# Optimization experiments

Measured on AMD Instinct MI355X. Metric: run time of the kernel, lower is better.

## Reference

```python
import jax, jax.numpy as jnp
import numpy as np


def _samx_row(qqq, kkk, vvv):
    """Suffix-automaton qkv retrieval over binary alphabet {0,1}.
    Faithful port of samx_qkv_slow, with dict transitions replaced by two
    flat transition arrays (alphabet size is 2 after the >0 binarization).
    """
    n = len(qqq)
    y = [0] * n
    s = 2 * n + 1
    tr = [[-1] * s, [-1] * s]   # tr[sym][state] = next state, -1 = absent
    f = [-1] * s                # suffix links
    m = [0] * s                 # max length of state
    r = [-1] * s                # last end position seen
    g = 0                       # last state
    u = 1                       # next free state id
    w = 0                       # current match state (query side)
    h = 0                       # current match length
    for i in range(n):
        q = qqq[i]
        k = kkk[i]
        tq = tr[q]
        tk = tr[k]
        # --- query: extend match with symbol q, following suffix links ---
        p, x = w, h
        while p != -1 and tq[p] == -1:
            if x > m[p]:
                x = m[p]
            p = f[p]
        if p != -1:
            p, x = tq[p], x + 1
        else:
            p, x = 0, 0
        # find tightest state for match length x
        vst = p
        while f[vst] != -1 and m[f[vst]] >= x:
            vst = f[vst]
        # back off to a state with positive length and a recorded endpos
        while vst != -1 and (m[vst] <= 0 or r[vst] < 0):
            vst = f[vst]
        yi = vvv[r[vst] + 1] if vst != -1 else -1
        y[i] = yi if yi > 0 else 0
        w, h = p, x
        # --- key: standard suffix-automaton extension with symbol k ---
        j = u
        u += 1
        m[j] = m[g] + 1
        p = g
        while p != -1 and tk[p] == -1:
            tk[p] = j
            p = f[p]
        if p == -1:
            f[j] = 0
        else:
            d = tk[p]
            if m[p] + 1 == m[d]:
                f[j] = d
            else:
                b = u
                u += 1
                tr[0][b] = tr[0][d]
                tr[1][b] = tr[1][d]
                m[b] = m[p] + 1
                f[b] = f[d]
                r[b] = r[d]
                f[d] = b
                f[j] = b
                while p != -1 and tk[p] == d:
                    tk[p] = b
                    p = f[p]
        # propagate latest end position up the suffix-link chain
        vst = g = j
        while vst != -1 and r[vst] < i:
            r[vst] = i
            vst = f[vst]
    return y


def _samx_idx(q, k, v):
    """q,k,v: float arrays [b,t,c] -> int idx [b,t,c] in {0,1}."""
    b, t, c = q.shape
    qb = (np.asarray(q) > 0).astype(np.uint8).transpose(0, 2, 1).reshape(-1, t)
    kb = (np.asarray(k) > 0).astype(np.uint8).transpose(0, 2, 1).reshape(-1, t)
    vb = (np.asarray(v) > 0).astype(np.uint8).transpose(0, 2, 1).reshape(-1, t)
    rows = [_samx_row(qq.tolist(), kk.tolist(), vv.tolist())
            for qq, kk, vv in zip(qb, kb, vb)]
    idx = np.asarray(rows, dtype=np.uint8).reshape(b, c, t).transpose(0, 2, 1)
    return idx


def setup_inputs() -> dict:
    key = jax.random.key(0)
    kq, kk, kv = jax.random.split(key, 3)
    B, T, C = 4, 2048, 256
    q = jax.random.normal(kq, (B, T, C), dtype=jnp.float32)
    k = jax.random.normal(kk, (B, T, C), dtype=jnp.float32)
    v = jax.random.normal(kv, (B, T, C), dtype=jnp.float32)
    e = jnp.ones((1, 1, C), dtype=jnp.float32)
    return {"q": q, "k": k, "v": v, "e": e}


def reference(q, k, v, e):
    # Irregular pointer-chasing part runs on host (numpy); output scaling in jnp.
    idx = _samx_idx(q, k, v)                      # [b,t,c] in {0,1}
    sign = 2.0 * jnp.asarray(idx, dtype=q.dtype) - 1.0
    return sign * e
```

## Files before the change

### kernel.cpp

```cpp
#include <hip/hip_runtime.h>


#define NSTATES 4096
#define TLEN 2048

typedef unsigned long long u64m;

__device__ __forceinline__ int f_tr(u64m r, int s) {
  return (int)(short)(unsigned short)(r >> (s << 4));
}
__device__ __forceinline__ int f_fl(u64m r) {
  return (int)(short)(unsigned short)(r >> 32);
}
__device__ __forceinline__ int f_ml(u64m r) {
  return (int)(r >> 48);
}

__device__ __forceinline__ int lane_shr1(int v, int lane) {
  int sh = __builtin_amdgcn_update_dpp(0, v, 0x111 , 0xF, 0xF, true);
  const int v15 = __builtin_amdgcn_readlane(v, 15);
  const int v31 = __builtin_amdgcn_readlane(v, 31);
  const int v47 = __builtin_amdgcn_readlane(v, 47);
  if (lane == 16) sh = v15;
  if (lane == 32) sh = v31;
  if (lane == 48) sh = v47;
  return sh;
}

__global__ __launch_bounds__(128)
void samx_main(const float* __restrict__ q,
               const float* __restrict__ k,
               unsigned* __restrict__ outpos,
               int T, int C) {
  __shared__ u64m           reca[NSTATES];
  __shared__ unsigned short rla[NSTATES];

  unsigned short* recw = (unsigned short*)reca;
  unsigned*       rech = (unsigned*)reca;

  const int row = blockIdx.x;
  const int b = row / C;
  const int c = row - b * C;
  const int lane = threadIdx.x & 63;
  const int wid = threadIdx.x >> 6;

  for (int s = threadIdx.x; s < NSTATES; s += 128) {
    reca[s] = 0x0000FFFFFFFFFFFFull;
    rla[s] = 0xFFFFu;
  }

  const size_t rowbase = (size_t)b * (size_t)T * (size_t)C + (size_t)c;
  unsigned* outr = outpos + rowbase;

  const float* src = (wid == 0 ? k : q) + rowbase;
  unsigned bits = 0u;
  {
    const int t0 = lane * 32;
#pragma unroll 8
    for (int jj = 0; jj < 32; ++jj) {
      if (src[(size_t)(t0 + jj) * C] > 0.0f) bits |= (1u << jj);
    }
  }
  __syncthreads();

  int cid = 0;
  bool cval = (lane == 0);
  bool trunc = false;
  int g = 0;
  int mlg = 0;
  int u = 1;
  int w = 0;
  int h = 0;

  int sym = (int)(__builtin_amdgcn_readlane((int)bits, 0) & 1);

  for (int i = 0; i < T; ++i) {
    const bool hot = !trunc;
    const int j = u++;
    const int mlj = mlg + 1;

    int d = -1, bb = -1, flj = 0, ndd = 0, newlen = 2, pushed = 0;
    bool prefl = false, inrun = false;

    if (wid == 0) {
      if (hot) {
        const int ks = sym;
        const u64m rk = reca[cid];
        const int img = f_tr(rk, ks);
        const int myml = f_ml(rk);
        const u64m brkmask = __ballot(cval && img != -1);
        const bool nobrk = (brkmask == 0);
        const int t2 = nobrk ? 64 : (int)__builtin_ctzll(brkmask);
        const int t2c = (t2 > 63) ? 63 : t2;
        d = __builtin_amdgcn_readlane(img, t2c);
        const int mlp = __builtin_amdgcn_readlane(myml, t2c);
        prefl = cval && (lane < t2);

        const u64m recd = reca[d < 0 ? 0 : d];

        const int previmg = lane_shr1(img, lane);
        const bool rs = cval && lane >= t2 && (lane == t2 || img != previmg);
        const u64m rsmask = __ballot(rs);
        ndd = (int)__builtin_popcountll(rsmask);
        newlen = ndd + 2;
        const unsigned below =
            __builtin_amdgcn_mbcnt_hi((unsigned)(rsmask >> 32),
                __builtin_amdgcn_mbcnt_lo((unsigned)rsmask, 0u));
        const int dst = rs ? ((int)below + 1) : 0;
        pushed = __builtin_amdgcn_ds_permute(dst << 2, img);

        int dtr0 = f_tr(recd, 0);
        int dtr1 = f_tr(recd, 1);
        const unsigned fmdhi = (unsigned)(recd >> 32);
        if (!nobrk) {
          const int mld = (int)(fmdhi >> 16);
          if (mlp + 1 == mld) {
            flj = d;
          } else {
            bb = u++;
            const u64m pb = __ballot(prefl && cid == d);
            if (pb != 0ull) { if (ks) dtr1 = j; else dtr0 = j; }
            if (lane == 0) {
              reca[bb] = (u64m)(unsigned short)dtr0
                       | ((u64m)(unsigned short)dtr1 << 16)
                       | ((u64m)(fmdhi & 0xFFFFu) << 32)
                       | ((u64m)(unsigned)(mlp + 1) << 48);
            }
            flj = bb;
          }
        }
        if (lane == 0)
          rech[2 * j + 1] = (unsigned)(flj & 0xFFFF) | ((unsigned)mlj << 16);

        if (bb >= 0) {
          const u64m eq = __ballot(cval && img == d) >> t2;
          const int runlen = (eq == ~0ull) ? 64 : (int)__builtin_ctzll(~eq);
          inrun = cval && lane >= t2 && lane < t2 + runlen;
        }
      }
    } else {
      const int qs = sym;
      int p = w, x = h;
      {
        u64m rr = reca[w];
        for (;;) {
          const int tv = f_tr(rr, qs);
          if (tv != -1) { p = tv; x = x + 1; break; }
          const int mp = f_ml(rr);
          if (x > mp) x = mp;
          p = f_fl(rr);
          if (p == -1) { p = 0; x = 0; break; }
          rr = reca[p];
        }
      }
      const u64m recP = reca[p];
      int rlv = (int)(short)rla[p];
      unsigned fmv = (unsigned)(recP >> 32);
      int vst = p;
      for (;;) {
        const int fv = (int)(short)(fmv & 0xFFFFu);
        if (fv == -1) break;
        const unsigned fmf = rech[2 * fv + 1];
        const int rlf = (int)(short)rla[fv];
        if ((int)(fmf >> 16) < x) break;
        vst = fv; fmv = fmf; rlv = rlf;
      }
      int rv = -1;
      for (;;) {
        if (vst == -1) { rv = -1; break; }
        if ((int)(fmv >> 16) > 0 && rlv >= 0) { rv = rlv; break; }
        vst = (int)(short)(fmv & 0xFFFFu);
        if (vst == -1) { rv = -1; break; }
        fmv = rech[2 * vst + 1];
        rlv = (int)(short)rla[vst];
      }
      w = p; h = x;
      if (lane == 0) outr[(size_t)i * C] = (unsigned)(rv + 1);
    }

    asm volatile("" ::: "memory");
    __builtin_amdgcn_s_barrier();
    asm volatile("" ::: "memory");

    if (wid == 0) {
      const int ks = sym;
      if (hot) {
        if (prefl) recw[4 * cid + ks] = (unsigned short)j;
        if (inrun) recw[4 * cid + ks] = (unsigned short)bb;
        if (bb >= 0 && lane == 0) recw[4 * d + 2] = (unsigned short)bb;

        int nv = 0;
        if (lane == 0) nv = j;
        else if (lane == 1) nv = flj;
        else if (lane - 1 < ndd) nv = pushed;
        const bool nval = (lane < newlen);
        if (nval) rla[nv] = (unsigned short)i;

        const bool overflow = (newlen > 64);
        if (overflow) {
          const int nv63 = __builtin_amdgcn_readlane(nv, 63);
          if (lane == 0) {
            int vp = (int)(short)(rech[2 * nv63 + 1] & 0xFFFFu);
            while (vp != -1) {
              rla[vp] = (unsigned short)i;
              vp = (int)(short)(rech[2 * vp + 1] & 0xFFFFu);
            }
          }
        }
        cid = nv; cval = nval; trunc = overflow;
      } else {
        int pcur = g, d2 = -1, idbrk = -1;
        for (;;) {
          if (pcur == -1) break;
          const u64m rr = reca[pcur];
          const int tv = f_tr(rr, ks);
          if (tv != -1) { d2 = tv; idbrk = pcur; break; }
          if (lane == 0) recw[4 * pcur + ks] = (unsigned short)j;
          pcur = f_fl(rr);
        }
        int fl2 = 0;
        if (d2 != -1) {
          const int mlp2 = f_ml(reca[idbrk]);
          const u64m rd2 = reca[d2];
          const int mld = f_ml(rd2);
          if (mlp2 + 1 == mld) {
            fl2 = d2;
          } else {
            const int bbc = u++;
            const int drl = (int)(short)rla[d2];
            if (lane == 0) {
              reca[bbc] = (u64m)(unsigned short)f_tr(rd2, 0)
                        | ((u64m)(unsigned short)f_tr(rd2, 1) << 16)
                        | ((u64m)((unsigned)(rd2 >> 32) & 0xFFFFu) << 32)
                        | ((u64m)(unsigned)(mlp2 + 1) << 48);
              rla[bbc] = (unsigned short)drl;
              recw[4 * d2 + 2] = (unsigned short)bbc;
            }
            fl2 = bbc;
            int p3 = idbrk;
            for (;;) {
              if (p3 == -1) break;
              const u64m r3 = reca[p3];
              const int tv3 = f_tr(r3, ks);
              if (tv3 != d2) break;
              if (lane == 0) recw[4 * p3 + ks] = (unsigned short)bbc;
              p3 = f_fl(r3);
            }
          }
        }
        if (lane == 0)
          rech[2 * j + 1] = (unsigned)(fl2 & 0xFFFF) | ((unsigned)mlj << 16);
        int vp = j, ncs = 0;
        bool tr2 = false;
        for (;;) {
          if (vp == -1) break;
          if (ncs < 64) { if (lane == ncs) cid = vp; ++ncs; }
          else tr2 = true;
          if (lane == 0) rla[vp] = (unsigned short)i;
          vp = (int)(short)(rech[2 * vp + 1] & 0xFFFFu);
        }
        cval = (lane < ncs);
        trunc = tr2;
      }
      g = j; mlg = mlj;
    }

    if (i + 1 < T) {
      const int in = i + 1;
      const unsigned bw = (unsigned)__builtin_amdgcn_readlane((int)bits, in >> 5);
      sym = (int)((bw >> (in & 31)) & 1u);
    }

    asm volatile("s_waitcnt lgkmcnt(0)" ::: "memory");
    __builtin_amdgcn_s_barrier();
    asm volatile("" ::: "memory");
  }
}

__global__ __launch_bounds__(256)
void samx_epilogue(const float* __restrict__ v,
                   const float* __restrict__ e,
                   unsigned* __restrict__ out,
                   int T, int C, int total) {
  const int idx = blockIdx.x * 256 + threadIdx.x;
  if (idx >= total) return;
  const unsigned vidx = out[idx];
  const int c = idx % C;
  const int bi = idx / C;
  const int b = bi / T;
  const float ev = e[c];
  float val = -ev;
  if (vidx != 0u) {
    if (v[((size_t)b * (size_t)T + (size_t)vidx) * (size_t)C + (size_t)c] > 0.0f)
      val = ev;
  }
  out[idx] = __float_as_uint(val);
}

extern "C" void kernel_launch(void* const* d_in, const int* in_sizes, int n_in,
                              void* d_out, int out_size, void* d_ws, size_t ws_size,
                              hipStream_t stream) {
  const float* q = (const float*)d_in[0];
  const float* k = (const float*)d_in[1];
  const float* v = (const float*)d_in[2];
  const float* e = (const float*)d_in[3];

  const int C = in_sizes[3];
  const int T = TLEN;
  const int B = in_sizes[0] / (T * C);
  const int total = out_size;

  samx_main<<<dim3(B * C), dim3(128), 0, stream>>>(q, k, (unsigned*)d_out, T, C);
  samx_epilogue<<<dim3((total + 255) / 256), dim3(256), 0, stream>>>(
      v, e, (unsigned*)d_out, T, C, total);
}
```

Measured before the change: 1.577 ms.

## Prefetch next-step automaton records and short-circuit break search via lane-1 record

The key wave now loads the next iteration's state record for its chain before the barrier, and keeps a register copy of the root state (rec0). When lane 1's successor record is known, it takes the transition break directly from that record, skipping the ballot/readlane search and the dependent LDS read of the break target. This aims to cut the serialized LDS latency on the per-step critical path. In exchange it adds extra register state and tracking logic that must stay consistent with the shared-memory records, especially after a clone or in the truncated (overflow) path.

```diff
diff --git a/kernel.cpp b/kernel.cpp
--- a/kernel.cpp
+++ b/kernel.cpp
@@ -14,6 +14,10 @@
 }
 __device__ __forceinline__ int f_ml(u64m r) {
   return (int)(r >> 48);
+}
+__device__ __forceinline__ u64m set_tr(u64m r, int s, int v) {
+  const int sh = s << 4;
+  return (r & ~(0xFFFFull << sh)) | ((u64m)(unsigned short)v << sh);
 }
 
 __device__ __forceinline__ int lane_shr1(int v, int lane) {
@@ -69,6 +73,12 @@
   int g = 0;
   int mlg = 0;
   int u = 1;
+  u64m rec0 = 0x0000FFFFFFFFFFFFull;
+  u64m pf_rec = reca[0];
+  u64m pf1c = 0;
+  u64m pf_recd = 0;
+  int  nx1 = -1;
+  bool have_pf1 = false;
   int w = 0;
   int h = 0;
 
@@ -80,23 +90,29 @@
     const int mlj = mlg + 1;
 
     int d = -1, bb = -1, flj = 0, ndd = 0, newlen = 2, pushed = 0;
-    bool prefl = false, inrun = false;
+    bool prefl = false, inrun = false, nobrk = false;
+    u64m pf1pre = 0;
 
     if (wid == 0) {
       if (hot) {
         const int ks = sym;
-        const u64m rk = reca[cid];
+        const u64m rk = pf_rec;
         const int img = f_tr(rk, ks);
-        const int myml = f_ml(rk);
-        const u64m brkmask = __ballot(cval && img != -1);
-        const bool nobrk = (brkmask == 0);
-        const int t2 = nobrk ? 64 : (int)__builtin_ctzll(brkmask);
-        const int t2c = (t2 > 63) ? 63 : t2;
-        d = __builtin_amdgcn_readlane(img, t2c);
-        const int mlp = __builtin_amdgcn_readlane(myml, t2c);
+        int t2, mlp;
+        u64m recd;
+        if (nx1 >= 0) {
+          t2 = 1; d = nx1; mlp = f_ml(pf1c); recd = pf_recd;
+        } else {
+          const int myml = f_ml(rk);
+          const u64m brkmask = __ballot(cval && img != -1);
+          nobrk = (brkmask == 0);
+          t2 = nobrk ? 64 : (int)__builtin_ctzll(brkmask);
+          const int t2c = (t2 > 63) ? 63 : t2;
+          d = __builtin_amdgcn_readlane(img, t2c);
+          mlp = __builtin_amdgcn_readlane(myml, t2c);
+          recd = reca[d < 0 ? 0 : d];
+        }
         prefl = cval && (lane < t2);
-
-        const u64m recd = reca[d < 0 ? 0 : d];
 
         const int previmg = lane_shr1(img, lane);
         const bool rs = cval && lane >= t2 && (lane == t2 || img != previmg);
@@ -116,15 +132,20 @@
           const int mld = (int)(fmdhi >> 16);
           if (mlp + 1 == mld) {
             flj = d;
+            pf1pre = (u64m)(unsigned short)dtr0
+                   | ((u64m)(unsigned short)dtr1 << 16)
+                   | ((u64m)(fmdhi & 0xFFFFu) << 32)
+                   | ((u64m)(unsigned)mld << 48);
           } else {
             bb = u++;
             const u64m pb = __ballot(prefl && cid == d);
             if (pb != 0ull) { if (ks) dtr1 = j; else dtr0 = j; }
+            pf1pre = (u64m)(unsigned short)dtr0
+                   | ((u64m)(unsigned short)dtr1 << 16)
+                   | ((u64m)(fmdhi & 0xFFFFu) << 32)
+                   | ((u64m)(unsigned)(mlp + 1) << 48);
             if (lane == 0) {
-              reca[bb] = (u64m)(unsigned short)dtr0
-                       | ((u64m)(unsigned short)dtr1 << 16)
-                       | ((u64m)(fmdhi & 0xFFFFu) << 32)
-                       | ((u64m)(unsigned)(mlp + 1) << 48);
+              reca[bb] = pf1pre;
             }
             flj = bb;
           }
@@ -182,12 +203,18 @@
     __builtin_amdgcn_s_barrier();
     asm volatile("" ::: "memory");
 
+    u64m pf1n = 0;
     if (wid == 0) {
       const int ks = sym;
       if (hot) {
         if (prefl) recw[4 * cid + ks] = (unsigned short)j;
         if (inrun) recw[4 * cid + ks] = (unsigned short)bb;
         if (bb >= 0 && lane == 0) recw[4 * d + 2] = (unsigned short)bb;
+
+        if (nobrk) rec0 = set_tr(rec0, ks, j);
+        else if (bb >= 0 && __ballot(inrun && cid == 0) != 0ull)
+          rec0 = set_tr(rec0, ks, bb);
+        pf1n = nobrk ? rec0 : pf1pre;
 
         int nv = 0;
         if (lane == 0) nv = j;
@@ -208,6 +235,7 @@
           }
         }
         cid = nv; cval = nval; trunc = overflow;
+        have_pf1 = !overflow;
       } else {
         int pcur = g, d2 = -1, idbrk = -1;
         for (;;) {
@@ -261,6 +289,8 @@
         }
         cval = (lane < ncs);
         trunc = tr2;
+        rec0 = reca[0];
+        have_pf1 = false;
       }
       g = j; mlg = mlj;
     }
@@ -271,7 +301,15 @@
       sym = (int)((bw >> (in & 31)) & 1u);
     }
 
-    asm volatile("s_waitcnt lgkmcnt(0)" ::: "memory");
+    if (wid == 0) {
+      asm volatile("s_waitcnt lgkmcnt(0)" ::: "memory");
+      if (i + 1 < T) {
+        pf_rec = reca[cid];
+        nx1 = have_pf1 ? f_tr(pf1n, sym) : -1;
+        pf_recd = reca[nx1 < 0 ? 0 : nx1];
+        pf1c = pf1n;
+      }
+    }
     __builtin_amdgcn_s_barrier();
     asm volatile("" ::: "memory");
   }
```

Measured after the change: 1.890 ms. 19.8% more time.

## Interleave two suffix-automaton rows per block with prefetched state records

Applied to the files above, without the earlier changes.

Each block now processes two independent rows in lock-step, with duplicated shared-memory automata, so the per-step barrier and LDS latency chains of one row overlap with the other's. It also prefetches the key-side current state record before the barrier, and adds a fast path on the query side that reuses the previously loaded record when it has not changed. The grid is halved. This doubles LDS use per block, which may lower occupancy, and relies on B*C being even.

```diff
diff --git a/kernel.cpp b/kernel.cpp
--- a/kernel.cpp
+++ b/kernel.cpp
@@ -32,150 +32,192 @@
                const float* __restrict__ k,
                unsigned* __restrict__ outpos,
                int T, int C) {
-  __shared__ u64m           reca[NSTATES];
-  __shared__ unsigned short rla[NSTATES];
-
-  unsigned short* recw = (unsigned short*)reca;
-  unsigned*       rech = (unsigned*)reca;
-
-  const int row = blockIdx.x;
-  const int b = row / C;
-  const int c = row - b * C;
+  __shared__ u64m           reca[2][NSTATES];
+  __shared__ unsigned short rla[2][NSTATES];
+
+  unsigned short* recwv[2] = {(unsigned short*)&reca[0][0],
+                              (unsigned short*)&reca[1][0]};
+  unsigned*       rechv[2] = {(unsigned*)&reca[0][0],
+                              (unsigned*)&reca[1][0]};
+
   const int lane = threadIdx.x & 63;
   const int wid = threadIdx.x >> 6;
 
   for (int s = threadIdx.x; s < NSTATES; s += 128) {
-    reca[s] = 0x0000FFFFFFFFFFFFull;
-    rla[s] = 0xFFFFu;
+    reca[0][s] = 0x0000FFFFFFFFFFFFull;
+    reca[1][s] = 0x0000FFFFFFFFFFFFull;
+    rla[0][s] = 0xFFFFu;
+    rla[1][s] = 0xFFFFu;
   }
 
-  const size_t rowbase = (size_t)b * (size_t)T * (size_t)C + (size_t)c;
-  unsigned* outr = outpos + rowbase;
-
-  const float* src = (wid == 0 ? k : q) + rowbase;
-  unsigned bits = 0u;
+  size_t rowbase[2];
+  unsigned* outr[2];
+  unsigned bits[2] = {0u, 0u};
   {
-    const int t0 = lane * 32;
+    const float* srcb = (wid == 0) ? k : q;
+#pragma unroll
+    for (int r = 0; r < 2; ++r) {
+      const int row = blockIdx.x * 2 + r;
+      const int b = row / C;
+      const int c = row - b * C;
+      rowbase[r] = (size_t)b * (size_t)T * (size_t)C + (size_t)c;
+      outr[r] = outpos + rowbase[r];
+      const float* src = srcb + rowbase[r];
+      const int t0 = lane * 32;
 #pragma unroll 8
-    for (int jj = 0; jj < 32; ++jj) {
-      if (src[(size_t)(t0 + jj) * C] > 0.0f) bits |= (1u << jj);
+      for (int jj = 0; jj < 32; ++jj) {
+        if (src[(size_t)(t0 + jj) * C] > 0.0f) bits[r] |= (1u << jj);
+      }
     }
   }
   __syncthreads();
 
-  int cid = 0;
-  bool cval = (lane == 0);
-  bool trunc = false;
-  int g = 0;
-  int mlg = 0;
-  int u = 1;
-  int w = 0;
-  int h = 0;
-
-  int sym = (int)(__builtin_amdgcn_readlane((int)bits, 0) & 1);
+  int  cid[2]  = {0, 0};
+  bool cval[2] = {lane == 0, lane == 0};
+  bool trunc[2] = {false, false};
+  int  g[2] = {0, 0}, mlg[2] = {0, 0}, uu[2] = {1, 1};
+  u64m pf_rec[2] = {reca[0][0], reca[1][0]};
+  int  w[2] = {0, 0}, h[2] = {0, 0};
+  u64m rrP[2] = {reca[0][0], reca[1][0]};
+
+  int symv[2];
+#pragma unroll
+  for (int r = 0; r < 2; ++r)
+    symv[r] = (int)(__builtin_amdgcn_readlane((int)bits[r], 0) & 1);
 
   for (int i = 0; i < T; ++i) {
-    const bool hot = !trunc;
-    const int j = u++;
-    const int mlj = mlg + 1;
-
-    int d = -1, bb = -1, flj = 0, ndd = 0, newlen = 2, pushed = 0;
-    bool prefl = false, inrun = false;
+    bool hot[2]; int jj[2], mljv[2];
+#pragma unroll
+    for (int r = 0; r < 2; ++r) {
+      hot[r] = !trunc[r];
+      jj[r] = uu[r]++;
+      mljv[r] = mlg[r] + 1;
+    }
+
+    int d[2] = {-1, -1}, bb[2] = {-1, -1}, flj[2] = {0, 0};
+    int ndd[2] = {0, 0}, newlen[2] = {2, 2}, pushed[2] = {0, 0};
+    int t2v[2] = {64, 64}, mlp[2] = {0, 0}, imgv[2] = {-1, -1};
+    bool prefl[2] = {false, false}, inrun[2] = {false, false};
+    bool nobrk[2] = {false, false};
+    u64m recd[2] = {0, 0};
 
     if (wid == 0) {
-      if (hot) {
-        const int ks = sym;
-        const u64m rk = reca[cid];
-        const int img = f_tr(rk, ks);
+#pragma unroll
+      for (int r = 0; r < 2; ++r) if (hot[r]) {
+        const int ks = symv[r];
+        const u64m rk = pf_rec[r];
+        imgv[r] = f_tr(rk, ks);
         const int myml = f_ml(rk);
-        const u64m brkmask = __ballot(cval && img != -1);
-        const bool nobrk = (brkmask == 0);
-        const int t2 = nobrk ? 64 : (int)__builtin_ctzll(brkmask);
-        const int t2c = (t2 > 63) ? 63 : t2;
-        d = __builtin_amdgcn_readlane(img, t2c);
-        const int mlp = __builtin_amdgcn_readlane(myml, t2c);
-        prefl = cval && (lane < t2);
-
-        const u64m recd = reca[d < 0 ? 0 : d];
-
-        const int previmg = lane_shr1(img, lane);
-        const bool rs = cval && lane >= t2 && (lane == t2 || img != previmg);
+        const u64m brkmask = __ballot(cval[r] && imgv[r] != -1);
+        nobrk[r] = (brkmask == 0);
+        t2v[r] = nobrk[r] ? 64 : (int)__builtin_ctzll(brkmask);
+        const int t2c = (t2v[r] > 63) ? 63 : t2v[r];
+        d[r] = __builtin_amdgcn_readlane(imgv[r], t2c);
+        mlp[r] = __builtin_amdgcn_readlane(myml, t2c);
+        prefl[r] = cval[r] && (lane < t2v[r]);
+
+        recd[r] = reca[r][d[r] < 0 ? 0 : d[r]];
+
+        const int previmg = lane_shr1(imgv[r], lane);
+        const bool rs = cval[r] && lane >= t2v[r] &&
+                        (lane == t2v[r] || imgv[r] != previmg);
         const u64m rsmask = __ballot(rs);
-        ndd = (int)__builtin_popcountll(rsmask);
-        newlen = ndd + 2;
+        ndd[r] = (int)__builtin_popcountll(rsmask);
+        newlen[r] = ndd[r] + 2;
         const unsigned below =
             __builtin_amdgcn_mbcnt_hi((unsigned)(rsmask >> 32),
                 __builtin_amdgcn_mbcnt_lo((unsigned)rsmask, 0u));
         const int dst = rs ? ((int)below + 1) : 0;
-        pushed = __builtin_amdgcn_ds_permute(dst << 2, img);
-
-        int dtr0 = f_tr(recd, 0);
-        int dtr1 = f_tr(recd, 1);
-        const unsigned fmdhi = (unsigned)(recd >> 32);
-        if (!nobrk) {
+        pushed[r] = __builtin_amdgcn_ds_permute(dst << 2, imgv[r]);
+      }
+#pragma unroll
+      for (int r = 0; r < 2; ++r) if (hot[r]) {
+        const int ks = symv[r];
+        int dtr0 = f_tr(recd[r], 0);
+        int dtr1 = f_tr(recd[r], 1);
+        const unsigned fmdhi = (unsigned)(recd[r] >> 32);
+        if (!nobrk[r]) {
           const int mld = (int)(fmdhi >> 16);
-          if (mlp + 1 == mld) {
-            flj = d;
+          if (mlp[r] + 1 == mld) {
+            flj[r] = d[r];
           } else {
-            bb = u++;
-            const u64m pb = __ballot(prefl && cid == d);
-            if (pb != 0ull) { if (ks) dtr1 = j; else dtr0 = j; }
+            bb[r] = uu[r]++;
+            const u64m pb = __ballot(prefl[r] && cid[r] == d[r]);
+            if (pb != 0ull) { if (ks) dtr1 = jj[r]; else dtr0 = jj[r]; }
             if (lane == 0) {
-              reca[bb] = (u64m)(unsigned short)dtr0
-                       | ((u64m)(unsigned short)dtr1 << 16)
-                       | ((u64m)(fmdhi & 0xFFFFu) << 32)
-                       | ((u64m)(unsigned)(mlp + 1) << 48);
+              reca[r][bb[r]] = (u64m)(unsigned short)dtr0
+                             | ((u64m)(unsigned short)dtr1 << 16)
+                             | ((u64m)(fmdhi & 0xFFFFu) << 32)
+                             | ((u64m)(unsigned)(mlp[r] + 1) << 48);
             }
-            flj = bb;
+            flj[r] = bb[r];
           }
         }
         if (lane == 0)
-          rech[2 * j + 1] = (unsigned)(flj & 0xFFFF) | ((unsigned)mlj << 16);
-
-        if (bb >= 0) {
-          const u64m eq = __ballot(cval && img == d) >> t2;
+          rechv[r][2 * jj[r] + 1] =
+              (unsigned)(flj[r] & 0xFFFF) | ((unsigned)mljv[r] << 16);
+
+        if (bb[r] >= 0) {
+          const u64m eq = __ballot(cval[r] && imgv[r] == d[r]) >> t2v[r];
           const int runlen = (eq == ~0ull) ? 64 : (int)__builtin_ctzll(~eq);
-          inrun = cval && lane >= t2 && lane < t2 + runlen;
+          inrun[r] = cval[r] && lane >= t2v[r] && lane < t2v[r] + runlen;
         }
       }
     } else {
-      const int qs = sym;
-      int p = w, x = h;
-      {
-        u64m rr = reca[w];
+      u64m fresh[2], rr2[2]; int rl2[2], tvs[2];
+#pragma unroll
+      for (int r = 0; r < 2; ++r) {
+        const int qs = symv[r];
+        fresh[r] = reca[r][w[r]];
+        tvs[r] = f_tr(rrP[r], qs);
+        const int ps = (tvs[r] != -1) ? tvs[r] : 0;
+        rr2[r] = reca[r][ps];
+        rl2[r] = (int)(short)rla[r][ps];
+      }
+#pragma unroll
+      for (int r = 0; r < 2; ++r) {
+        const int qs = symv[r];
+        int p, x;
+        u64m recP; int rlv;
+        if (fresh[r] == rrP[r] && tvs[r] != -1) {
+          p = tvs[r]; x = h[r] + 1; recP = rr2[r]; rlv = rl2[r];
+        } else {
+          u64m rr = fresh[r]; p = w[r]; x = h[r];
+          for (;;) {
+            const int tv = f_tr(rr, qs);
+            if (tv != -1) { p = tv; x = x + 1; break; }
+            const int mp = f_ml(rr);
+            if (x > mp) x = mp;
+            p = f_fl(rr);
+            if (p == -1) { p = 0; x = 0; break; }
+            rr = reca[r][p];
+          }
+          recP = reca[r][p]; rlv = (int)(short)rla[r][p];
+        }
+
+        unsigned fmv = (unsigned)(recP >> 32);
+        int vst = p;
         for (;;) {
-          const int tv = f_tr(rr, qs);
-          if (tv != -1) { p = tv; x = x + 1; break; }
-          const int mp = f_ml(rr);
-          if (x > mp) x = mp;
-          p = f_fl(rr);
-          if (p == -1) { p = 0; x = 0; break; }
-          rr = reca[p];
-        }
-      }
-      const u64m recP = reca[p];
-      int rlv = (int)(short)rla[p];
-      unsigned fmv = (unsigned)(recP >> 32);
-      int vst = p;
-      for (;;) {
-        const int fv = (int)(short)(fmv & 0xFFFFu);
-        if (fv == -1) break;
-        const unsigned fmf = rech[2 * fv + 1];
-        const int rlf = (int)(short)rla[fv];
-        if ((int)(fmf >> 16) < x) break;
-        vst = fv; fmv = fmf; rlv = rlf;
-      }
-      int rv = -1;
-      for (;;) {
-        if (vst == -1) { rv = -1; break; }
-        if ((int)(fmv >> 16) > 0 && rlv >= 0) { rv = rlv; break; }
-        vst = (int)(short)(fmv & 0xFFFFu);
-        if (vst == -1) { rv = -1; break; }
-        fmv = rech[2 * vst + 1];
-        rlv = (int)(short)rla[vst];
-      }
-      w = p; h = x;
-      if (lane == 0) outr[(size_t)i * C] = (unsigned)(rv + 1);
+          const int fv = (int)(short)(fmv & 0xFFFFu);
+          if (fv == -1) break;
+          const unsigned fmf = rechv[r][2 * fv + 1];
+          const int rlf = (int)(short)rla[r][fv];
+          if ((int)(fmf >> 16) < x) break;
+          vst = fv; fmv = fmf; rlv = rlf;
+        }
+        int rv = -1;
+        for (;;) {
+          if (vst == -1) { rv = -1; break; }
+          if ((int)(fmv >> 16) > 0 && rlv >= 0) { rv = rlv; break; }
+          vst = (int)(short)(fmv & 0xFFFFu);
+          if (vst == -1) { rv = -1; break; }
+          fmv = rechv[r][2 * vst + 1];
+          rlv = (int)(short)rla[r][vst];
+        }
+        w[r] = p; h[r] = x;
+        rrP[r] = recP;
+        if (lane == 0) outr[r][(size_t)i * C] = (unsigned)(rv + 1);
+      }
     }
 
     asm volatile("" ::: "memory");
@@ -183,95 +225,108 @@
     asm volatile("" ::: "memory");
 
     if (wid == 0) {
-      const int ks = sym;
-      if (hot) {
-        if (prefl) recw[4 * cid + ks] = (unsigned short)j;
-        if (inrun) recw[4 * cid + ks] = (unsigned short)bb;
-        if (bb >= 0 && lane == 0) recw[4 * d + 2] = (unsigned short)bb;
-
-        int nv = 0;
-        if (lane == 0) nv = j;
-        else if (lane == 1) nv = flj;
-        else if (lane - 1 < ndd) nv = pushed;
-        const bool nval = (lane < newlen);
-        if (nval) rla[nv] = (unsigned short)i;
-
-        const bool overflow = (newlen > 64);
-        if (overflow) {
-          const int nv63 = __builtin_amdgcn_readlane(nv, 63);
-          if (lane == 0) {
-            int vp = (int)(short)(rech[2 * nv63 + 1] & 0xFFFFu);
-            while (vp != -1) {
-              rla[vp] = (unsigned short)i;
-              vp = (int)(short)(rech[2 * vp + 1] & 0xFFFFu);
+#pragma unroll
+      for (int r = 0; r < 2; ++r) {
+        const int ks = symv[r];
+        if (hot[r]) {
+          if (prefl[r]) recwv[r][4 * cid[r] + ks] = (unsigned short)jj[r];
+          if (inrun[r]) recwv[r][4 * cid[r] + ks] = (unsigned short)bb[r];
+          if (bb[r] >= 0 && lane == 0)
+            recwv[r][4 * d[r] + 2] = (unsigned short)bb[r];
+
+          int nv = 0;
+          if (lane == 0) nv = jj[r];
+          else if (lane == 1) nv = flj[r];
+          else if (lane - 1 < ndd[r]) nv = pushed[r];
+          const bool nval = (lane < newlen[r]);
+          if (nval) rla[r][nv] = (unsigned short)i;
+
+          const bool overflow = (newlen[r] > 64);
+          if (overflow) {
+            const int nv63 = __builtin_amdgcn_readlane(nv, 63);
+            if (lane == 0) {
+              int vp = (int)(short)(rechv[r][2 * nv63 + 1] & 0xFFFFu);
+              while (vp != -1) {
+                rla[r][vp] = (unsigned short)i;
+                vp = (int)(short)(rechv[r][2 * vp + 1] & 0xFFFFu);
+              }
             }
           }
-        }
-        cid = nv; cval = nval; trunc = overflow;
-      } else {
-        int pcur = g, d2 = -1, idbrk = -1;
-        for (;;) {
-          if (pcur == -1) break;
-          const u64m rr = reca[pcur];
-          const int tv = f_tr(rr, ks);
-          if (tv != -1) { d2 = tv; idbrk = pcur; break; }
-          if (lane == 0) recw[4 * pcur + ks] = (unsigned short)j;
-          pcur = f_fl(rr);
-        }
-        int fl2 = 0;
-        if (d2 != -1) {
-          const int mlp2 = f_ml(reca[idbrk]);
-          const u64m rd2 = reca[d2];
-          const int mld = f_ml(rd2);
-          if (mlp2 + 1 == mld) {
-            fl2 = d2;
-          } else {
-            const int bbc = u++;
-            const int drl = (int)(short)rla[d2];
-            if (lane == 0) {
-              reca[bbc] = (u64m)(unsigned short)f_tr(rd2, 0)
-                        | ((u64m)(unsigned short)f_tr(rd2, 1) << 16)
-                        | ((u64m)((unsigned)(rd2 >> 32) & 0xFFFFu) << 32)
-                        | ((u64m)(unsigned)(mlp2 + 1) << 48);
-              rla[bbc] = (unsigned short)drl;
-              recw[4 * d2 + 2] = (unsigned short)bbc;
+          cid[r] = nv; cval[r] = nval; trunc[r] = overflow;
+        } else {
+          int pcur = g[r], d2 = -1, idbrk = -1;
+          for (;;) {
+            if (pcur == -1) break;
+            const u64m rr = reca[r][pcur];
+            const int tv = f_tr(rr, ks);
+            if (tv != -1) { d2 = tv; idbrk = pcur; break; }
+            if (lane == 0) recwv[r][4 * pcur + ks] = (unsigned short)jj[r];
+            pcur = f_fl(rr);
+          }
+          int fl2 = 0;
+          if (d2 != -1) {
+            const int mlp2 = f_ml(reca[r][idbrk]);
+            const u64m rd2 = reca[r][d2];
+            const int mld = f_ml(rd2);
+            if (mlp2 + 1 == mld) {
+              fl2 = d2;
+            } else {
+              const int bbc = uu[r]++;
+              const int drl = (int)(short)rla[r][d2];
+              if (lane == 0) {
+                reca[r][bbc] = (u64m)(unsigned short)f_tr(rd2, 0)
+                             | ((u64m)(unsigned short)f_tr(rd2, 1) << 16)
+                             | ((u64m)((unsigned)(rd2 >> 32) & 0xFFFFu) << 32)
+                             | ((u64m)(unsigned)(mlp2 + 1) << 48);
+                rla[r][bbc] = (unsigned short)drl;
+                recwv[r][4 * d2 + 2] = (unsigned short)bbc;
+              }
+              fl2 = bbc;
+              int p3 = idbrk;
+              for (;;) {
+                if (p3 == -1) break;
+                const u64m r3 = reca[r][p3];
+                const int tv3 = f_tr(r3, ks);
+                if (tv3 != d2) break;
+                if (lane == 0) recwv[r][4 * p3 + ks] = (unsigned short)bbc;
+                p3 = f_fl(r3);
+              }
             }
-            fl2 = bbc;
-            int p3 = idbrk;
-            for (;;) {
-              if (p3 == -1) break;
-              const u64m r3 = reca[p3];
-              const int tv3 = f_tr(r3, ks);
-              if (tv3 != d2) break;
-              if (lane == 0) recw[4 * p3 + ks] = (unsigned short)bbc;
-              p3 = f_fl(r3);
-            }
-          }
-        }
-        if (lane == 0)
-          rech[2 * j + 1] = (unsigned)(fl2 & 0xFFFF) | ((unsigned)mlj << 16);
-        int vp = j, ncs = 0;
-        bool tr2 = false;
-        for (;;) {
-          if (vp == -1) break;
-          if (ncs < 64) { if (lane == ncs) cid = vp; ++ncs; }
-          else tr2 = true;
-          if (lane == 0) rla[vp] = (unsigned short)i;
-          vp = (int)(short)(rech[2 * vp + 1] & 0xFFFFu);
-        }
-        cval = (lane < ncs);
-        trunc = tr2;
-      }
-      g = j; mlg = mlj;
+          }
+          if (lane == 0)
+            rechv[r][2 * jj[r] + 1] =
+                (unsigned)(fl2 & 0xFFFF) | ((unsigned)mljv[r] << 16);
+          int vp = jj[r], ncs = 0;
+          bool tr2 = false;
+          for (;;) {
+            if (vp == -1) break;
+            if (ncs < 64) { if (lane == ncs) cid[r] = vp; ++ncs; }
+            else tr2 = true;
+            if (lane == 0) rla[r][vp] = (unsigned short)i;
+            vp = (int)(short)(rechv[r][2 * vp + 1] & 0xFFFFu);
+          }
+          cval[r] = (lane < ncs);
+          trunc[r] = tr2;
+        }
+        g[r] = jj[r]; mlg[r] = mljv[r];
+      }
     }
 
     if (i + 1 < T) {
       const int in = i + 1;
-      const unsigned bw = (unsigned)__builtin_amdgcn_readlane((int)bits, in >> 5);
-      sym = (int)((bw >> (in & 31)) & 1u);
+#pragma unroll
+      for (int r = 0; r < 2; ++r) {
+        const unsigned bw =
+            (unsigned)__builtin_amdgcn_readlane((int)bits[r], in >> 5);
+        symv[r] = (int)((bw >> (in & 31)) & 1u);
+      }
     }
 
     asm volatile("s_waitcnt lgkmcnt(0)" ::: "memory");
+    if (wid == 0 && i + 1 < T) {
+      pf_rec[0] = reca[0][cid[0]];
+      pf_rec[1] = reca[1][cid[1]];
+    }
     __builtin_amdgcn_s_barrier();
     asm volatile("" ::: "memory");
   }
@@ -310,7 +365,8 @@
   const int B = in_sizes[0] / (T * C);
   const int total = out_size;
 
-  samx_main<<<dim3(B * C), dim3(128), 0, stream>>>(q, k, (unsigned*)d_out, T, C);
+  samx_main<<<dim3((B * C) / 2), dim3(128), 0, stream>>>(
+      q, k, (unsigned*)d_out, T, C);
   samx_epilogue<<<dim3((total + 255) / 256), dim3(256), 0, stream>>>(
       v, e, (unsigned*)d_out, T, C, total);
 }
```

New measurement: 3.148 ms. 99.6% more time.
